# Optimization experiments

Measured on AMD Instinct MI355X. Metric: run time of the kernel, lower is better.

Reference implementation:

```python
import jax, jax.numpy as jnp
import numpy as np

D_MODEL = 1024
NHEAD = 16
HEAD_DIM = D_MODEL // NHEAD


def setup_inputs() -> dict:
    key = jax.random.key(0)
    k_x, k_wqkv, k_bqkv, k_wo, k_bo = jax.random.split(key, 5)
    scale_in = 1.0 / np.sqrt(D_MODEL)
    x = jax.random.normal(k_x, (2, 2048, D_MODEL), dtype=jnp.float32)
    # qkv_proj: Linear(d_model, 3*d_model); stored as [in, out] for x @ W
    W_qkv = jax.random.uniform(k_wqkv, (D_MODEL, 3 * D_MODEL), dtype=jnp.float32,
                               minval=-scale_in, maxval=scale_in)
    b_qkv = jax.random.uniform(k_bqkv, (3 * D_MODEL,), dtype=jnp.float32,
                               minval=-scale_in, maxval=scale_in)
    W_out = jax.random.uniform(k_wo, (D_MODEL, D_MODEL), dtype=jnp.float32,
                               minval=-scale_in, maxval=scale_in)
    b_out = jax.random.uniform(k_bo, (D_MODEL,), dtype=jnp.float32,
                               minval=-scale_in, maxval=scale_in)
    return {"x": x, "W_qkv": W_qkv, "b_qkv": b_qkv, "W_out": W_out, "b_out": b_out}


def reference(x, W_qkv, b_qkv, W_out, b_out):
    B, S, _ = x.shape
    qkv = x @ W_qkv + b_qkv                                   # [B,S,3*d_model]
    # Faithful to torch module: reshape to [B,S,H,3*hd], move heads, chunk LAST dim
    qkv = qkv.reshape(B, S, NHEAD, 3 * HEAD_DIM)
    qkv = qkv.transpose(0, 2, 1, 3)                            # [B,H,S,3*hd]
    q, k, v = jnp.split(qkv, 3, axis=-1)                       # each [B,H,S,hd]
    scale = 1.0 / np.sqrt(HEAD_DIM).astype(np.float32)
    attn = jnp.einsum('bhqd,bhkd->bhqk', q, k) * scale         # [B,H,S,S]
    attn = jax.nn.softmax(attn, axis=-1)
    out = jnp.einsum('bhqk,bhkd->bhqd', attn, v)               # [B,H,S,hd]
    out = out.transpose(0, 2, 1, 3).reshape(B, S, D_MODEL)     # [B,S,d_model]
    return out @ W_out + b_out
```

## Files before the change

### kernel.cpp

```cpp
#include <hip/hip_runtime.h>
#include <cmath>

typedef unsigned short u16;
typedef unsigned int u32;
typedef __bf16 bf16x8 __attribute__((ext_vector_type(8)));
typedef float f32x4 __attribute__((ext_vector_type(4)));

#define D_MODEL 1024
#define NHEAD 16
#define HD 64
#define SEQ 2048
#define BATCH 2
#define M_TOK 4096
#define N_QKV 3072

#define LOG2E 1.4426950408889634f
#define SOFTMAX_SHIFT 11.541560327111707f

__device__ __forceinline__ u16 f2bf(float f) {
    u32 u = __float_as_uint(f);
    u32 r = (u + 0x7fffu + ((u >> 16) & 1u)) >> 16;
    return (u16)r;
}

__device__ __forceinline__ float bf2f(u16 v) {
    return __uint_as_float(((u32)v) << 16);
}

__device__ __forceinline__ u32 pack_bf(float a, float b) {
#if __has_builtin(__builtin_amdgcn_cvt_pk_bf16_f32)
    typedef __bf16 bf16x2_t __attribute__((ext_vector_type(2)));
    union { bf16x2_t v; u32 u; } c;
    c.v = __builtin_amdgcn_cvt_pk_bf16_f32(a, b);
    return c.u;
#else
    u32 ua = __float_as_uint(a) + 0x8000u;
    u32 ub = __float_as_uint(b) + 0x8000u;
    return __builtin_amdgcn_perm(ub, ua, 0x07060302u);
#endif
}

__device__ __forceinline__ bf16x8 ld_bf8(const u16* p) {
    return *(const bf16x8*)p;
}

__device__ __forceinline__ bf16x8 as_bf8(int4 v) {
    union { int4 i; bf16x8 b; } u; u.i = v; return u.b;
}

__device__ __forceinline__ f32x4 mfma16(bf16x8 a, bf16x8 b, f32x4 c) {
    return __builtin_amdgcn_mfma_f32_16x16x32_bf16(a, b, c, 0, 0, 0);
}

__device__ __forceinline__ void gload_lds16(const u16* g, u16* l) {
    __builtin_amdgcn_global_load_lds(
        (const __attribute__((address_space(1))) void*)g,
        (__attribute__((address_space(3))) void*)l, 16, 0, 0);
}

__device__ __forceinline__ int Gv(int x) {
    int q = x / 192, rm = x - q * 192;
    int e = rm - 128;
    return q * 64 + (e > 0 ? e : 0);
}

__device__ __forceinline__ void transpose_body(
    const float* __restrict__ in, u16* __restrict__ out,
    int rows, int cols, int bx, int by, float (*tile)[33])
{
    int c0 = bx * 32;
    int r0 = by * 32;
    int tx = threadIdx.x & 31;
    int ty = threadIdx.x >> 5;
#pragma unroll
    for (int i = 0; i < 32; i += 8)
        tile[ty + i][tx] = in[(size_t)(r0 + ty + i) * cols + c0 + tx];
    __syncthreads();
#pragma unroll
    for (int i = 0; i < 32; i += 8)
        out[(size_t)(c0 + ty + i) * rows + r0 + tx] = f2bf(tile[tx][ty + i]);
}

__global__ __launch_bounds__(256) void prep_kernel(
    const float* __restrict__ x, u16* __restrict__ Xb,
    const float* __restrict__ Wqkv, u16* __restrict__ Wqkvt,
    const float* __restrict__ Wout, u16* __restrict__ Woutt)
{
    __shared__ float tile[32][33];
    int b = blockIdx.x;
    if (b < 1024) {
        int n4 = M_TOK * D_MODEL / 4;
        int i = b * 256 + threadIdx.x;
        int stride = 1024 * 256;
        for (; i < n4; i += stride) {
            float4 v = ((const float4*)x)[i];
            ushort4 o;
            o.x = f2bf(v.x); o.y = f2bf(v.y); o.z = f2bf(v.z); o.w = f2bf(v.w);
            ((ushort4*)Xb)[i] = o;
        }
    } else if (b < 1024 + 3072) {
        int bb = b - 1024;
        transpose_body(Wqkv, Wqkvt, 1024, 3072, bb % 96, bb / 96, tile);
    } else {
        int bb = b - 4096;
        transpose_body(Wout, Woutt, 1024, 1024, bb % 32, bb / 32, tile);
    }
}

__global__ __launch_bounds__(256) void gemm_qkv_kernel(
    const u16* __restrict__ A, const u16* __restrict__ Bt, const float* __restrict__ bias,
    u16* __restrict__ Qb, u16* __restrict__ Kb, u16* __restrict__ Vp)
{
    __shared__ u16 lA[128 * 32];
    __shared__ u16 lB[128 * 32];
    __shared__ u16 vtile[64 * 132];
    int w = threadIdx.x >> 6, l = threadIdx.x & 63;
    int col = l & 15, quad = l >> 4;
    int wm = w >> 1, wn = w & 1;
    int m0 = blockIdx.x * 128;
    int n0 = blockIdx.y * 128;
    int lrow = l >> 2;
    int lcol = (l & 3) * 8;

    f32x4 acc[4][4] = {};
    for (int k0 = 0; k0 < 1024; k0 += 32) {
        __syncthreads();
#pragma unroll
        for (int i = 0; i < 2; i++) {
            int slab = w * 32 + i * 16;
            gload_lds16(A  + (size_t)(m0 + slab + lrow) * 1024 + k0 + lcol, lA + slab * 32);
            gload_lds16(Bt + (size_t)(n0 + slab + lrow) * 1024 + k0 + lcol, lB + slab * 32);
        }
        __syncthreads();
        bf16x8 af[4], bfr[4];
#pragma unroll
        for (int i = 0; i < 4; i++)
            af[i] = ld_bf8(lA + (wm * 64 + i * 16 + col) * 32 + quad * 8);
#pragma unroll
        for (int j = 0; j < 4; j++)
            bfr[j] = ld_bf8(lB + (wn * 64 + j * 16 + col) * 32 + quad * 8);
#pragma unroll
        for (int i = 0; i < 4; i++)
#pragma unroll
            for (int j = 0; j < 4; j++)
                acc[i][j] = mfma16(af[i], bfr[j], acc[i][j]);
    }

    int s0 = m0 & 2047;
    int bblk = m0 >> 11;
#pragma unroll
    for (int i = 0; i < 4; i++) {
#pragma unroll
        for (int j = 0; j < 4; j++) {
            int cc = n0 + wn * 64 + j * 16 + col;
            int h = cc / 192;
            int within = cc - h * 192;
            int ww = within >> 6;
            int d = within & 63;
            int vloc = Gv(cc) - Gv(n0);
            float bv = bias[cc];
#pragma unroll
            for (int r = 0; r < 4; r++) {
                int sloc = wm * 64 + i * 16 + quad * 4 + r;
                int s = s0 + sloc;
                int bh = bblk * NHEAD + h;
                float val = acc[i][j][r] + bv;
                if (ww == 0)      Qb[(size_t)(bh * SEQ + s) * HD + d] = f2bf(val * 0.125f);
                else if (ww == 1) Kb[(size_t)(bh * SEQ + s) * HD + d] = f2bf(val);
                else {
                    int sp = (sloc & ~31) | ((sloc & 12) << 1) | (((sloc >> 4) & 1) << 2) | (sloc & 3);
                    vtile[vloc * 132 + sp] = f2bf(val);
                }
            }
        }
    }
    __syncthreads();
    int vcols = Gv(n0 + 128) - Gv(n0);
    int gbase = Gv(n0);
    for (int c = threadIdx.x; c < vcols * 16; c += 256) {
        int vloc = c >> 4, gi = c & 15;
        int av = gbase + vloc;
        int h = av >> 6, d = av & 63;
        int bh = bblk * NHEAD + h;
        int4 vv = *(const int4*)(vtile + vloc * 132 + gi * 8);
        *(int4*)(Vp + ((size_t)(bh * HD + d)) * SEQ + s0 + gi * 8) = vv;
    }
}

__global__ __launch_bounds__(256, 2) void attn_kernel(
    const u16* __restrict__ Qb, const u16* __restrict__ Kb,
    const u16* __restrict__ Vp, u16* __restrict__ O0,
    u16* __restrict__ O1, float* __restrict__ Lp)
{
    __shared__ u16 kbuf[2][64 * 64];
    __shared__ u16 vbuf[2][64 * 64];
    int wave = threadIdx.x >> 6, lane = threadIdx.x & 63;
    int col = lane & 15, quad = lane >> 4;
    int g = blockIdx.x;
    int xcd = g & 7, slot = g >> 3;
    int bh = xcd * 4 + (slot >> 4);
    int rem = slot & 15;
    int split = rem >> 3;
    int qt = rem & 7;
    int q0 = qt * 256 + wave * 64;
    int kstart = split * 16;

    int srow = lane >> 3;
    int sgrp = (lane & 7) ^ srow;
    const u16* Kt0 = Kb + (size_t)bh * SEQ * HD;
    const u16* Vt0 = Vp + (size_t)bh * HD * SEQ;
    long soffK = (long)srow * HD + sgrp * 8;
    long soffV = (long)srow * SEQ + sgrp * 8;
    int r0 = wave * 16;

    int rbase = col * 64;
    int sw0 = ((quad)     ^ (col & 7)) * 8;
    int sw1 = ((quad + 4) ^ (col & 7)) * 8;

    union { u32 w[4]; int4 i; } onesu;
    onesu.w[0] = onesu.w[1] = onesu.w[2] = onesu.w[3] = 0x3F803F80u;
    bf16x8 ones = as_bf8(onesu.i);

    f32x4 zf = {};

    bf16x8 aq[4][2];
#pragma unroll
    for (int m = 0; m < 4; m++) {
        const u16* qbase = Qb + ((size_t)bh * SEQ + q0 + m * 16 + col) * HD + quad * 8;
        aq[m][0] = ld_bf8(qbase);
        aq[m][1] = ld_bf8(qbase + 32);
    }

    f32x4 o[4][4] = {};
    f32x4 ol[4] = {};

    {
        int kbase = kstart * 64;
        gload_lds16(Kt0 + (size_t)(kbase + r0) * HD + soffK,      kbuf[0] + r0 * 64);
        gload_lds16(Kt0 + (size_t)(kbase + r0 + 8) * HD + soffK,  kbuf[0] + (r0 + 8) * 64);
        gload_lds16(Vt0 + (size_t)r0 * SEQ + kbase + soffV,       vbuf[0] + r0 * 64);
        gload_lds16(Vt0 + (size_t)(r0 + 8) * SEQ + kbase + soffV, vbuf[0] + (r0 + 8) * 64);
    }

    for (int kt = 0; kt < 16; ++kt) {
        int cur = kt & 1;
        __syncthreads();
        if (kt + 1 < 16) {
            int kbase = (kstart + kt + 1) * 64;
            int nb = cur ^ 1;
            gload_lds16(Kt0 + (size_t)(kbase + r0) * HD + soffK,      kbuf[nb] + r0 * 64);
            gload_lds16(Kt0 + (size_t)(kbase + r0 + 8) * HD + soffK,  kbuf[nb] + (r0 + 8) * 64);
            gload_lds16(Vt0 + (size_t)r0 * SEQ + kbase + soffV,       vbuf[nb] + r0 * 64);
            gload_lds16(Vt0 + (size_t)(r0 + 8) * SEQ + kbase + soffV, vbuf[nb] + (r0 + 8) * 64);
        }
        const u16* kb = kbuf[cur];
        const u16* vb = vbuf[cur];
        bf16x8 kf[4][2];
#pragma unroll
        for (int t = 0; t < 4; t++) {
            kf[t][0] = ld_bf8(kb + t * 1024 + rbase + sw0);
            kf[t][1] = ld_bf8(kb + t * 1024 + rbase + sw1);
        }
        int4 vraw[4][2];
#pragma unroll
        for (int t = 0; t < 4; t++) {
            vraw[t][0] = *(const int4*)(vb + t * 1024 + rbase + sw0);
            vraw[t][1] = *(const int4*)(vb + t * 1024 + rbase + sw1);
        }
#pragma unroll
        for (int m = 0; m < 4; m++) {
            f32x4 sa[4];
            __builtin_amdgcn_s_setprio(1);
#pragma unroll
            for (int t = 0; t < 4; t++) {
                sa[t] = mfma16(kf[t][0], aq[m][0], zf);
                sa[t] = mfma16(kf[t][1], aq[m][1], sa[t]);
            }
            __builtin_amdgcn_s_setprio(0);
            int4 pfrag[2];
#pragma unroll
            for (int t = 0; t < 4; t++) {
                f32x4 p;
#pragma unroll
                for (int r = 0; r < 4; r++)
                    p[r] = __builtin_exp2f(__builtin_fmaf(sa[t][r], LOG2E, -SOFTMAX_SHIFT));
                u32 lo = pack_bf(p[0], p[1]);
                u32 hi = pack_bf(p[2], p[3]);
                if ((t & 1) == 0) { pfrag[t >> 1].x = (int)lo; pfrag[t >> 1].y = (int)hi; }
                else              { pfrag[t >> 1].z = (int)lo; pfrag[t >> 1].w = (int)hi; }
            }
            __builtin_amdgcn_s_setprio(1);
#pragma unroll
            for (int t = 0; t < 4; t++)
#pragma unroll
                for (int h = 0; h < 2; h++)
                    o[m][t] = mfma16(as_bf8(pfrag[h]), as_bf8(vraw[t][h]), o[m][t]);
            ol[m] = mfma16(as_bf8(pfrag[0]), ones, ol[m]);
            ol[m] = mfma16(as_bf8(pfrag[1]), ones, ol[m]);
            __builtin_amdgcn_s_setprio(0);
        }
    }

    u16* Op = split ? O1 : O0;
#pragma unroll
    for (int m = 0; m < 4; m++) {
#pragma unroll
        for (int r = 0; r < 4; r++) {
            int srow2 = q0 + m * 16 + quad * 4 + r;
            if (col == 0)
                Lp[(size_t)split * 32 * SEQ + (size_t)bh * SEQ + srow2] = ol[m][r];
#pragma unroll
            for (int t = 0; t < 4; t++)
                Op[((size_t)bh * SEQ + srow2) * HD + t * 16 + col] = f2bf(o[m][t][r]);
        }
    }
}

__global__ __launch_bounds__(256) void combine_kernel(
    const u16* __restrict__ O0, const u16* __restrict__ O1,
    const float* __restrict__ Lp, u16* __restrict__ At)
{
    int i = blockIdx.x * 256 + threadIdx.x;
    int dg = i & 15;
    int q = (i >> 4) & 2047;
    int bh = i >> 15;
    size_t ob = ((size_t)bh * SEQ + q) * HD + dg * 4;
    ushort4 a = *(const ushort4*)(O0 + ob);
    ushort4 b = *(const ushort4*)(O1 + ob);
    float l = Lp[(size_t)bh * SEQ + q] + Lp[(size_t)32 * SEQ + (size_t)bh * SEQ + q];
    float inv = 1.f / l;
    int bb = bh >> 4, h = bh & 15;
    ushort4 o;
    o.x = f2bf((bf2f(a.x) + bf2f(b.x)) * inv);
    o.y = f2bf((bf2f(a.y) + bf2f(b.y)) * inv);
    o.z = f2bf((bf2f(a.z) + bf2f(b.z)) * inv);
    o.w = f2bf((bf2f(a.w) + bf2f(b.w)) * inv);
    *(ushort4*)(At + ((size_t)(bb * SEQ + q)) * D_MODEL + h * 64 + dg * 4) = o;
}

__global__ __launch_bounds__(256) void gemm_out_kernel(
    const u16* __restrict__ A, const u16* __restrict__ Bt, const float* __restrict__ bias,
    float* __restrict__ out)
{
    __shared__ u16 lA[128 * 32];
    __shared__ u16 lB[128 * 32];
    int w = threadIdx.x >> 6, l = threadIdx.x & 63;
    int col = l & 15, quad = l >> 4;
    int wm = w >> 1, wn = w & 1;
    int m0 = blockIdx.x * 128;
    int n0 = blockIdx.y * 128;
    int lrow = l >> 2;
    int lcol = (l & 3) * 8;

    f32x4 acc[4][4] = {};
    for (int k0 = 0; k0 < 1024; k0 += 32) {
        __syncthreads();
#pragma unroll
        for (int i = 0; i < 2; i++) {
            int slab = w * 32 + i * 16;
            gload_lds16(A  + (size_t)(m0 + slab + lrow) * 1024 + k0 + lcol, lA + slab * 32);
            gload_lds16(Bt + (size_t)(n0 + slab + lrow) * 1024 + k0 + lcol, lB + slab * 32);
        }
        __syncthreads();
        bf16x8 af[4], bfr[4];
#pragma unroll
        for (int i = 0; i < 4; i++)
            af[i] = ld_bf8(lA + (wm * 64 + i * 16 + col) * 32 + quad * 8);
#pragma unroll
        for (int j = 0; j < 4; j++)
            bfr[j] = ld_bf8(lB + (wn * 64 + j * 16 + col) * 32 + quad * 8);
#pragma unroll
        for (int i = 0; i < 4; i++)
#pragma unroll
            for (int j = 0; j < 4; j++)
                acc[i][j] = mfma16(af[i], bfr[j], acc[i][j]);
    }

#pragma unroll
    for (int i = 0; i < 4; i++) {
#pragma unroll
        for (int j = 0; j < 4; j++) {
            int cc = n0 + wn * 64 + j * 16 + col;
            float bv = bias[cc];
#pragma unroll
            for (int r = 0; r < 4; r++) {
                int row = m0 + wm * 64 + i * 16 + quad * 4 + r;
                out[(size_t)row * D_MODEL + cc] = acc[i][j][r] + bv;
            }
        }
    }
}

extern "C" void kernel_launch(void* const* d_in, const int* in_sizes, int n_in,
                              void* d_out, int out_size, void* d_ws, size_t ws_size,
                              hipStream_t stream) {
    const float* x     = (const float*)d_in[0];
    const float* W_qkv = (const float*)d_in[1];
    const float* b_qkv = (const float*)d_in[2];
    const float* W_out = (const float*)d_in[3];
    const float* b_out = (const float*)d_in[4];
    float* out = (float*)d_out;

    char* ws = (char*)d_ws;
    u16* Xb    = (u16*)(ws);
    u16* Wqkvt = (u16*)(ws + (8ull << 20));
    u16* Qb    = (u16*)(ws + (16ull << 20));
    u16* Kb    = (u16*)(ws + (24ull << 20));
    u16* Vp    = (u16*)(ws + (32ull << 20));
    u16* O0    = (u16*)(ws);
    u16* O1    = (u16*)(ws + (8ull << 20));
    float* Lp  = (float*)(ws + (40ull << 20));
    u16* At    = (u16*)(ws + (16ull << 20));
    u16* Woutt = (u16*)(ws + (41ull << 20));

    prep_kernel<<<dim3(5120), 256, 0, stream>>>(x, Xb, W_qkv, Wqkvt, W_out, Woutt);
    gemm_qkv_kernel<<<dim3(32, 24), 256, 0, stream>>>(Xb, Wqkvt, b_qkv, Qb, Kb, Vp);
    attn_kernel<<<dim3(512), 256, 0, stream>>>(Qb, Kb, Vp, O0, O1, Lp);
    combine_kernel<<<dim3(BATCH * NHEAD * SEQ * (HD / 4) / 256), 256, 0, stream>>>(O0, O1, Lp, At);
    gemm_out_kernel<<<dim3(32, 8), 256, 0, stream>>>(At, Woutt, b_out, out);
}
```

Measured before the change: 202.8 us.

## Split attention KV range four ways and reduce partials with float atomics

The attention kernel now splits each head's key range into four chunks instead of two, launching twice as many blocks. It also raises the occupancy hint in launch bounds from 2 to 4 blocks per CU. Instead of each split writing its own bf16 partial output and row sum, every split atomically adds fp32 partial outputs and row sums into zeroed global buffers, cleared by two memsets. The combine kernel then just normalizes one fp32 buffer. This buys more parallelism and occupancy at the cost of many global atomics, extra memset traffic, larger fp32 intermediates, and possible register spills under the tighter register budget.

```diff
diff --git a/kernel.cpp b/kernel.cpp
--- a/kernel.cpp
+++ b/kernel.cpp
@@ -187,10 +187,10 @@
     }
 }
 
-__global__ __launch_bounds__(256, 2) void attn_kernel(
+__global__ __launch_bounds__(256, 4) void attn_kernel(
     const u16* __restrict__ Qb, const u16* __restrict__ Kb,
-    const u16* __restrict__ Vp, u16* __restrict__ O0,
-    u16* __restrict__ O1, float* __restrict__ Lp)
+    const u16* __restrict__ Vp, float* __restrict__ Of,
+    float* __restrict__ Lf)
 {
     __shared__ u16 kbuf[2][64 * 64];
     __shared__ u16 vbuf[2][64 * 64];
@@ -198,12 +198,12 @@
     int col = lane & 15, quad = lane >> 4;
     int g = blockIdx.x;
     int xcd = g & 7, slot = g >> 3;
-    int bh = xcd * 4 + (slot >> 4);
-    int rem = slot & 15;
+    int bh = xcd * 4 + (slot >> 5);
+    int rem = slot & 31;
     int split = rem >> 3;
     int qt = rem & 7;
     int q0 = qt * 256 + wave * 64;
-    int kstart = split * 16;
+    int kstart = split * 8;
 
     int srow = lane >> 3;
     int sgrp = (lane & 7) ^ srow;
@@ -242,10 +242,10 @@
         gload_lds16(Vt0 + (size_t)(r0 + 8) * SEQ + kbase + soffV, vbuf[0] + (r0 + 8) * 64);
     }
 
-    for (int kt = 0; kt < 16; ++kt) {
+    for (int kt = 0; kt < 8; ++kt) {
         int cur = kt & 1;
         __syncthreads();
-        if (kt + 1 < 16) {
+        if (kt + 1 < 8) {
             int kbase = (kstart + kt + 1) * 64;
             int nb = cur ^ 1;
             gload_lds16(Kt0 + (size_t)(kbase + r0) * HD + soffK,      kbuf[nb] + r0 * 64);
@@ -301,40 +301,36 @@
         }
     }
 
-    u16* Op = split ? O1 : O0;
 #pragma unroll
     for (int m = 0; m < 4; m++) {
 #pragma unroll
         for (int r = 0; r < 4; r++) {
             int srow2 = q0 + m * 16 + quad * 4 + r;
             if (col == 0)
-                Lp[(size_t)split * 32 * SEQ + (size_t)bh * SEQ + srow2] = ol[m][r];
+                atomicAdd(&Lf[(size_t)bh * SEQ + srow2], ol[m][r]);
 #pragma unroll
             for (int t = 0; t < 4; t++)
-                Op[((size_t)bh * SEQ + srow2) * HD + t * 16 + col] = f2bf(o[m][t][r]);
+                atomicAdd(&Of[((size_t)bh * SEQ + srow2) * HD + t * 16 + col], o[m][t][r]);
         }
     }
 }
 
 __global__ __launch_bounds__(256) void combine_kernel(
-    const u16* __restrict__ O0, const u16* __restrict__ O1,
-    const float* __restrict__ Lp, u16* __restrict__ At)
+    const float* __restrict__ Of, const float* __restrict__ Lf, u16* __restrict__ At)
 {
     int i = blockIdx.x * 256 + threadIdx.x;
     int dg = i & 15;
     int q = (i >> 4) & 2047;
     int bh = i >> 15;
     size_t ob = ((size_t)bh * SEQ + q) * HD + dg * 4;
-    ushort4 a = *(const ushort4*)(O0 + ob);
-    ushort4 b = *(const ushort4*)(O1 + ob);
-    float l = Lp[(size_t)bh * SEQ + q] + Lp[(size_t)32 * SEQ + (size_t)bh * SEQ + q];
-    float inv = 1.f / l;
+    float4 a = *(const float4*)(Of + ob);
+    float inv = 1.f / Lf[(size_t)bh * SEQ + q];
     int bb = bh >> 4, h = bh & 15;
     ushort4 o;
-    o.x = f2bf((bf2f(a.x) + bf2f(b.x)) * inv);
-    o.y = f2bf((bf2f(a.y) + bf2f(b.y)) * inv);
-    o.z = f2bf((bf2f(a.z) + bf2f(b.z)) * inv);
-    o.w = f2bf((bf2f(a.w) + bf2f(b.w)) * inv);
+    o.x = f2bf(a.x * inv);
+    o.y = f2bf(a.y * inv);
+    o.z = f2bf(a.z * inv);
+    o.w = f2bf(a.w * inv);
     *(ushort4*)(At + ((size_t)(bb * SEQ + q)) * D_MODEL + h * 64 + dg * 4) = o;
 }
 
@@ -407,15 +403,16 @@
     u16* Qb    = (u16*)(ws + (16ull << 20));
     u16* Kb    = (u16*)(ws + (24ull << 20));
     u16* Vp    = (u16*)(ws + (32ull << 20));
-    u16* O0    = (u16*)(ws);
-    u16* O1    = (u16*)(ws + (8ull << 20));
-    float* Lp  = (float*)(ws + (40ull << 20));
+    float* Of  = (float*)(ws);
+    float* Lf  = (float*)(ws + (40ull << 20));
     u16* At    = (u16*)(ws + (16ull << 20));
     u16* Woutt = (u16*)(ws + (41ull << 20));
 
     prep_kernel<<<dim3(5120), 256, 0, stream>>>(x, Xb, W_qkv, Wqkvt, W_out, Woutt);
     gemm_qkv_kernel<<<dim3(32, 24), 256, 0, stream>>>(Xb, Wqkvt, b_qkv, Qb, Kb, Vp);
-    attn_kernel<<<dim3(512), 256, 0, stream>>>(Qb, Kb, Vp, O0, O1, Lp);
-    combine_kernel<<<dim3(BATCH * NHEAD * SEQ * (HD / 4) / 256), 256, 0, stream>>>(O0, O1, Lp, At);
+    hipMemsetAsync(Of, 0, (size_t)32 * SEQ * HD * sizeof(float), stream);
+    hipMemsetAsync(Lf, 0, (size_t)32 * SEQ * sizeof(float), stream);
+    attn_kernel<<<dim3(1024), 256, 0, stream>>>(Qb, Kb, Vp, Of, Lf);
+    combine_kernel<<<dim3(BATCH * NHEAD * SEQ * (HD / 4) / 256), 256, 0, stream>>>(Of, Lf, At);
     gemm_out_kernel<<<dim3(32, 8), 256, 0, stream>>>(At, Woutt, b_out, out);
 }
```

New measurement: 372.2 us. 1.83x slower.

## Split attention key range across two wave groups per block and fold softmax scale into Q

Applied to the files above, without the earlier changes.

The attention block grows to 512 threads, forming two groups of four waves. Each group processes half of the block's key tiles in its own double-buffered LDS region, and the partial outputs and row sums are reduced through shared memory before one write. Separately, the log2e factor is folded into the Q scaling in the QKV GEMM and the fixed softmax shift is dropped, which saves an FMA per exponent. This doubles the waves working on each query tile and raises occupancy. In exchange it adds an in-block reduction with a bf16 round-trip of the partial outputs, and drops the overflow shift, so large scores could overflow exp2.

```diff
diff --git a/kernel.cpp b/kernel.cpp
--- a/kernel.cpp
+++ b/kernel.cpp
@@ -15,7 +15,7 @@
 #define N_QKV 3072
 
 #define LOG2E 1.4426950408889634f
-#define SOFTMAX_SHIFT 11.541560327111707f
+#define Q_SCALE 0.18033688011112042f
 
 __device__ __forceinline__ u16 f2bf(float f) {
     u32 u = __float_as_uint(f);
@@ -165,7 +165,7 @@
                 int s = s0 + sloc;
                 int bh = bblk * NHEAD + h;
                 float val = acc[i][j][r] + bv;
-                if (ww == 0)      Qb[(size_t)(bh * SEQ + s) * HD + d] = f2bf(val * 0.125f);
+                if (ww == 0)      Qb[(size_t)(bh * SEQ + s) * HD + d] = f2bf(val * Q_SCALE);
                 else if (ww == 1) Kb[(size_t)(bh * SEQ + s) * HD + d] = f2bf(val);
                 else {
                     int sp = (sloc & ~31) | ((sloc & 12) << 1) | (((sloc >> 4) & 1) << 2) | (sloc & 3);
@@ -187,23 +187,25 @@
     }
 }
 
-__global__ __launch_bounds__(256, 2) void attn_kernel(
+__global__ __launch_bounds__(512, 4) void attn_kernel(
     const u16* __restrict__ Qb, const u16* __restrict__ Kb,
     const u16* __restrict__ Vp, u16* __restrict__ O0,
     u16* __restrict__ O1, float* __restrict__ Lp)
 {
-    __shared__ u16 kbuf[2][64 * 64];
-    __shared__ u16 vbuf[2][64 * 64];
+    __shared__ u16 kbuf[2][2][64 * 64];
+    __shared__ u16 vbuf[2][2][64 * 64];
+    __shared__ float lexch[4][64];
     int wave = threadIdx.x >> 6, lane = threadIdx.x & 63;
+    int wl = wave & 3, grp = wave >> 2;
     int col = lane & 15, quad = lane >> 4;
     int g = blockIdx.x;
     int xcd = g & 7, slot = g >> 3;
     int bh = xcd * 4 + (slot >> 4);
     int rem = slot & 15;
-    int split = rem >> 3;
+    int osplit = rem >> 3;
     int qt = rem & 7;
-    int q0 = qt * 256 + wave * 64;
-    int kstart = split * 16;
+    int q0 = qt * 256 + wl * 64;
+    int kstart = osplit * 16 + grp * 8;
 
     int srow = lane >> 3;
     int sgrp = (lane & 7) ^ srow;
@@ -211,7 +213,7 @@
     const u16* Vt0 = Vp + (size_t)bh * HD * SEQ;
     long soffK = (long)srow * HD + sgrp * 8;
     long soffV = (long)srow * SEQ + sgrp * 8;
-    int r0 = wave * 16;
+    int r0 = wl * 16;
 
     int rbase = col * 64;
     int sw0 = ((quad)     ^ (col & 7)) * 8;
@@ -236,25 +238,25 @@
 
     {
         int kbase = kstart * 64;
-        gload_lds16(Kt0 + (size_t)(kbase + r0) * HD + soffK,      kbuf[0] + r0 * 64);
-        gload_lds16(Kt0 + (size_t)(kbase + r0 + 8) * HD + soffK,  kbuf[0] + (r0 + 8) * 64);
-        gload_lds16(Vt0 + (size_t)r0 * SEQ + kbase + soffV,       vbuf[0] + r0 * 64);
-        gload_lds16(Vt0 + (size_t)(r0 + 8) * SEQ + kbase + soffV, vbuf[0] + (r0 + 8) * 64);
-    }
-
-    for (int kt = 0; kt < 16; ++kt) {
+        gload_lds16(Kt0 + (size_t)(kbase + r0) * HD + soffK,      kbuf[grp][0] + r0 * 64);
+        gload_lds16(Kt0 + (size_t)(kbase + r0 + 8) * HD + soffK,  kbuf[grp][0] + (r0 + 8) * 64);
+        gload_lds16(Vt0 + (size_t)r0 * SEQ + kbase + soffV,       vbuf[grp][0] + r0 * 64);
+        gload_lds16(Vt0 + (size_t)(r0 + 8) * SEQ + kbase + soffV, vbuf[grp][0] + (r0 + 8) * 64);
+    }
+
+    for (int kt = 0; kt < 8; ++kt) {
         int cur = kt & 1;
         __syncthreads();
-        if (kt + 1 < 16) {
+        if (kt + 1 < 8) {
             int kbase = (kstart + kt + 1) * 64;
             int nb = cur ^ 1;
-            gload_lds16(Kt0 + (size_t)(kbase + r0) * HD + soffK,      kbuf[nb] + r0 * 64);
-            gload_lds16(Kt0 + (size_t)(kbase + r0 + 8) * HD + soffK,  kbuf[nb] + (r0 + 8) * 64);
-            gload_lds16(Vt0 + (size_t)r0 * SEQ + kbase + soffV,       vbuf[nb] + r0 * 64);
-            gload_lds16(Vt0 + (size_t)(r0 + 8) * SEQ + kbase + soffV, vbuf[nb] + (r0 + 8) * 64);
-        }
-        const u16* kb = kbuf[cur];
-        const u16* vb = vbuf[cur];
+            gload_lds16(Kt0 + (size_t)(kbase + r0) * HD + soffK,      kbuf[grp][nb] + r0 * 64);
+            gload_lds16(Kt0 + (size_t)(kbase + r0 + 8) * HD + soffK,  kbuf[grp][nb] + (r0 + 8) * 64);
+            gload_lds16(Vt0 + (size_t)r0 * SEQ + kbase + soffV,       vbuf[grp][nb] + r0 * 64);
+            gload_lds16(Vt0 + (size_t)(r0 + 8) * SEQ + kbase + soffV, vbuf[grp][nb] + (r0 + 8) * 64);
+        }
+        const u16* kb = kbuf[grp][cur];
+        const u16* vb = vbuf[grp][cur];
         bf16x8 kf[4][2];
 #pragma unroll
         for (int t = 0; t < 4; t++) {
@@ -283,7 +285,7 @@
                 f32x4 p;
 #pragma unroll
                 for (int r = 0; r < 4; r++)
-                    p[r] = __builtin_exp2f(__builtin_fmaf(sa[t][r], LOG2E, -SOFTMAX_SHIFT));
+                    p[r] = __builtin_exp2f(sa[t][r]);
                 u32 lo = pack_bf(p[0], p[1]);
                 u32 hi = pack_bf(p[2], p[3]);
                 if ((t & 1) == 0) { pfrag[t >> 1].x = (int)lo; pfrag[t >> 1].y = (int)hi; }
@@ -301,17 +303,40 @@
         }
     }
 
-    u16* Op = split ? O1 : O0;
-#pragma unroll
-    for (int m = 0; m < 4; m++) {
-#pragma unroll
-        for (int r = 0; r < 4; r++) {
-            int srow2 = q0 + m * 16 + quad * 4 + r;
-            if (col == 0)
-                Lp[(size_t)split * 32 * SEQ + (size_t)bh * SEQ + srow2] = ol[m][r];
-#pragma unroll
-            for (int t = 0; t < 4; t++)
-                Op[((size_t)bh * SEQ + srow2) * HD + t * 16 + col] = f2bf(o[m][t][r]);
+    __syncthreads();
+    u16* ex = (wl < 2) ? &kbuf[1][wl][0] : &vbuf[1][wl - 2][0];
+    if (grp == 1) {
+#pragma unroll
+        for (int m = 0; m < 4; m++) {
+#pragma unroll
+            for (int r = 0; r < 4; r++) {
+                int rr = m * 16 + quad * 4 + r;
+                if (col == 0)
+                    lexch[wl][rr] = ol[m][r];
+#pragma unroll
+                for (int t = 0; t < 4; t++)
+                    ex[rr * 64 + t * 16 + col] = f2bf(o[m][t][r]);
+            }
+        }
+    }
+    __syncthreads();
+    if (grp == 0) {
+        u16* Op = osplit ? O1 : O0;
+#pragma unroll
+        for (int m = 0; m < 4; m++) {
+#pragma unroll
+            for (int r = 0; r < 4; r++) {
+                int rr = m * 16 + quad * 4 + r;
+                int srow2 = q0 + rr;
+                if (col == 0)
+                    Lp[(size_t)osplit * 32 * SEQ + (size_t)bh * SEQ + srow2] =
+                        ol[m][r] + lexch[wl][rr];
+#pragma unroll
+                for (int t = 0; t < 4; t++) {
+                    float v = o[m][t][r] + bf2f(ex[rr * 64 + t * 16 + col]);
+                    Op[((size_t)bh * SEQ + srow2) * HD + t * 16 + col] = f2bf(v);
+                }
+            }
         }
     }
 }
@@ -415,7 +440,7 @@
 
     prep_kernel<<<dim3(5120), 256, 0, stream>>>(x, Xb, W_qkv, Wqkvt, W_out, Woutt);
     gemm_qkv_kernel<<<dim3(32, 24), 256, 0, stream>>>(Xb, Wqkvt, b_qkv, Qb, Kb, Vp);
-    attn_kernel<<<dim3(512), 256, 0, stream>>>(Qb, Kb, Vp, O0, O1, Lp);
+    attn_kernel<<<dim3(512), 512, 0, stream>>>(Qb, Kb, Vp, O0, O1, Lp);
     combine_kernel<<<dim3(BATCH * NHEAD * SEQ * (HD / 4) / 256), 256, 0, stream>>>(O0, O1, Lp, At);
     gemm_out_kernel<<<dim3(32, 8), 256, 0, stream>>>(At, Woutt, b_out, out);
 }
```

Measured after the change: 337.2 us. 66.3% more time.
